# Optimization experiments

Hardware: AMD Instinct MI355X
Metric: run time of the kernel (lower is better)

Reference implementation:

```python
import jax, jax.numpy as jnp
import numpy as np

NUM_USERS = 100000
NUM_ITEMS = 50000
N_NODES = NUM_USERS + NUM_ITEMS
N_INTERACTIONS = 1000000
LATENT_DIM = 32
K = 4
N_LAYERS = 3
BATCH = 4096


def setup_inputs() -> dict:
    key = jax.random.key(0)
    k_u, k_i = jax.random.split(key)
    # torch init: normal std=0.1
    user_emb = 0.1 * jax.random.normal(k_u, (NUM_USERS, LATENT_DIM * K), dtype=jnp.float32)
    item_emb = 0.1 * jax.random.normal(k_i, (NUM_ITEMS, LATENT_DIM * K), dtype=jnp.float32)
    # build symmetric normalized bipartite adjacency (LightGCN getSparseGraph)
    rng = np.random.default_rng(0)
    u = rng.integers(0, NUM_USERS, N_INTERACTIONS)
    it = rng.integers(0, NUM_ITEMS, N_INTERACTIONS)
    src = np.concatenate([u, it + NUM_USERS]).astype(np.int32)
    dst = np.concatenate([it + NUM_USERS, u]).astype(np.int32)
    deg = np.bincount(src, minlength=N_NODES).astype(np.float32)
    deg = np.maximum(deg, 1.0)
    val = (1.0 / np.sqrt(deg[src] * deg[dst])).astype(np.float32)
    users = rng.integers(0, NUM_USERS, BATCH).astype(np.int32)
    items = rng.integers(0, NUM_ITEMS, BATCH).astype(np.int32)
    return {
        "user_emb": user_emb,
        "item_emb": item_emb,
        "edge_src": jnp.asarray(src),
        "edge_dst": jnp.asarray(dst),
        "edge_val": jnp.asarray(val),
        "users": jnp.asarray(users),
        "items": jnp.asarray(items),
    }


def _computer(user_emb, item_emb, edge_src, edge_dst, edge_val):
    n_users = user_emb.shape[0]
    n = n_users + item_emb.shape[0]
    # [N, K, D] disentangled factor view of the K*D embedding
    x = jnp.concatenate([user_emb, item_emb], axis=0).reshape(n, K, -1)
    embs = [x]
    for _ in range(N_LAYERS):
        # SpMM over all K factor slices at once: out[dst] += val * x[src]
        msgs = x[edge_src] * edge_val[:, None, None]  # [E, K, D]
        x = jax.ops.segment_sum(msgs, edge_dst, num_segments=n)
        embs.append(x)
    light_out = jnp.mean(jnp.stack(embs, axis=1), axis=1)  # [N, K, D]
    return light_out[:n_users], light_out[n_users:]


def reference(user_emb, item_emb, edge_src, edge_dst, edge_val, users, items):
    all_users, all_items = _computer(user_emb, item_emb, edge_src, edge_dst, edge_val)
    u = all_users[users]   # [B, K, D]
    i = all_items[items]   # [B, K, D]
    return jnp.sum(u * i, axis=(-1, -2))  # [B]
```

## Files before the change

### kernel.cpp

```cpp
#include <hip/hip_runtime.h>

#define NUM_USERS 100000
#define NUM_ITEMS 50000
#define N_NODES   150000
#define N_EDGES   2000000
#define N_INTER   1000000
#define DIM       128
#define DIM4      32
#define BATCH     4096
#define B_SHIFT   9
#define BUCK_N    (1 << B_SHIFT)
#define NBUCK     ((N_NODES + BUCK_N - 1) >> B_SHIFT)
#define PAIRS     4096
#define NPBLK     ((N_INTER + PAIRS - 1) / PAIRS)
#define CAP       12288
#define CAPB      16384
#define MARK_BLOCKS 512
#define CONV_BLOCKS (((N_NODES + 1) * 8 + 255) / 256)

#define G0 16.0f
#define INV_G1 (1.0f / 64.0f)
#define INV_G2 (1.0f / 256.0f)

typedef __attribute__((ext_vector_type(4))) float f32x4;
typedef __attribute__((ext_vector_type(2))) float f32x2;

__device__ inline f32x2 f8x2_lo(unsigned w) { return __builtin_amdgcn_cvt_pk_f32_fp8(w, 0); }
__device__ inline f32x2 f8x2_hi(unsigned w) { return __builtin_amdgcn_cvt_pk_f32_fp8(w, 1); }
__device__ inline unsigned enc_lo(float a, float b, unsigned old) {
    return __builtin_amdgcn_cvt_pk_fp8_f32(a, b, old, 0);
}
__device__ inline unsigned enc_hi(float a, float b, unsigned old) {
    return __builtin_amdgcn_cvt_pk_fp8_f32(a, b, old, 1);
}

__device__ inline int scan512(int v, int t, int* wsum) {
    int incl = v;
#pragma unroll
    for (int off = 1; off < 64; off <<= 1) {
        int u = __shfl_up(incl, off, 64);
        if ((t & 63) >= off) incl += u;
    }
    __syncthreads();
    if ((t & 63) == 63) wsum[t >> 6] = incl;
    __syncthreads();
    int add = 0;
    int w = t >> 6;
    for (int k = 0; k < w; ++k) add += wsum[k];
    return incl + add;
}


__global__ void bucket_scatter_kernel(const int* __restrict__ src,
                                      int* __restrict__ bcur,
                                      int* __restrict__ tmp) {
    __shared__ int lhist[NBUCK];
    __shared__ int lcur[NBUCK];
    int t = threadIdx.x;
    int base = blockIdx.x * PAIRS;
    for (int i = t; i < NBUCK; i += 512) lhist[i] = 0;
    __syncthreads();
    for (int i = 0; i < PAIRS / 512; ++i) {
        int gp = base + i * 512 + t;
        if (gp < N_INTER) {
            int u = src[gp];
            int v = src[N_INTER + gp];
            atomicAdd(&lhist[v >> B_SHIFT], 1);
            atomicAdd(&lhist[u >> B_SHIFT], 1);
        }
    }
    __syncthreads();
    for (int i = t; i < NBUCK; i += 512) {
        int c = lhist[i];
        lcur[i] = c ? (i * CAPB + atomicAdd(&bcur[i], c)) : 0;
    }
    __syncthreads();
    for (int i = 0; i < PAIRS / 512; ++i) {
        int gp = base + i * 512 + t;
        if (gp < N_INTER) {
            int u = src[gp];
            int v = src[N_INTER + gp];
            int bv = v >> B_SHIFT;
            int bu = u >> B_SHIFT;
            int pos0 = atomicAdd(&lcur[bv], 1);
            if (pos0 < (bv + 1) * CAPB)
                tmp[pos0] = (u << B_SHIFT) | (v & (BUCK_N - 1));
            int pos1 = atomicAdd(&lcur[bu], 1);
            if (pos1 < (bu + 1) * CAPB)
                tmp[pos1] = (v << B_SHIFT) | (u & (BUCK_N - 1));
        }
    }
}


__global__ void place_kernel(const int* __restrict__ bcur,
                             const int* __restrict__ tmp,
                             int* __restrict__ row_start,
                             float* __restrict__ rinv,
                             float* __restrict__ sdeg,
                             int* __restrict__ csr_src) {
    __shared__ int lhist[BUCK_N];
    __shared__ int lofs[BUCK_N];
    __shared__ int ssc[512];
    __shared__ int wsum[8];
    __shared__ int outbuf[CAP];
    int b = blockIdx.x;
    int t = threadIdx.x;

    int c = 0;
    if (t < NBUCK) {
        c = bcur[t];
        if (c > CAPB) c = CAPB;
    }
    ssc[t] = scan512(c, t, wsum);
    __syncthreads();
    int beg = (b == 0) ? 0 : ssc[b - 1];
    int end = ssc[b];
    int cnt = end - beg;
    int tbase = b * CAPB;
    int n0 = b << B_SHIFT;
    int n1 = n0 + BUCK_N; if (n1 > N_NODES) n1 = N_NODES;
    if (b == NBUCK - 1 && t == 0) row_start[N_NODES] = end;

    lhist[t] = 0;
    __syncthreads();
    for (int e = t; e < cnt; e += 512)
        atomicAdd(&lhist[tmp[tbase + e] & (BUCK_N - 1)], 1);
    __syncthreads();

    int v = lhist[t];
    int incl = scan512(v, t, wsum);
    int excl = incl - v;
    lofs[t] = excl;
    int node = n0 + t;
    if (node < n1) {
        row_start[node] = beg + excl;
        float d = (float)(v > 1 ? v : 1);
        float rr = rsqrtf(d);
        rinv[node] = rr;
        sdeg[node] = d * rr;
    }
    __syncthreads();

    if (cnt <= CAP) {
        for (int e = t; e < cnt; e += 512) {
            int p = tmp[tbase + e];
            int pos = atomicAdd(&lofs[p & (BUCK_N - 1)], 1);
            outbuf[pos] = p >> B_SHIFT;
        }
        __syncthreads();
        for (int i = t; i < cnt; i += 512) csr_src[beg + i] = outbuf[i];
    } else {
        for (int e = t; e < cnt; e += 512) {
            int p = tmp[tbase + e];
            int pos = atomicAdd(&lofs[p & (BUCK_N - 1)], 1);
            csr_src[beg + pos] = p >> B_SHIFT;
        }
    }
}


__global__ void mark_conv_kernel(const f32x4* __restrict__ ue4,
                                 const f32x4* __restrict__ ie4,
                                 const float* __restrict__ rinv,
                                 uint4* __restrict__ e16f8,
                                 uint4* __restrict__ w1f8,
                                 uint4* __restrict__ w2f8,
                                 const int* __restrict__ users,
                                 const int* __restrict__ items,
                                 const int* __restrict__ row_start,
                                 const int* __restrict__ csr_src,
                                 int* __restrict__ mark) {
    int bid = blockIdx.x;
    if (bid < MARK_BLOCKS) {
        int g = threadIdx.x >> 4;
        int lane = threadIdx.x & 15;
        int b = bid * 16 + g;
        int node = (b < BATCH) ? users[b] : (NUM_USERS + items[b - BATCH]);
        if (lane == 0) mark[node] = 1;
        int beg = row_start[node], end = row_start[node + 1];
        for (int e = beg + lane; e < end; e += 16) mark[csr_src[e]] = 1;
        return;
    }
    int i = (bid - MARK_BLOCKS) * 256 + threadIdx.x;
    const int total = (N_NODES + 1) * 8;
    if (i >= total) return;
    int n = i >> 3;
    if (n >= N_NODES) {
        uint4 z = make_uint4(0u, 0u, 0u, 0u);
        e16f8[i] = z;
        w1f8[i] = z;
        w2f8[i] = z;
        return;
    }
    int j = i & 7;
    const f32x4* row = (n < NUM_USERS) ? ue4 + (size_t)n * DIM4
                                       : ie4 + (size_t)(n - NUM_USERS) * DIM4;
    float r = rinv[n] * G0;
    f32x4 c0 = __builtin_nontemporal_load(&row[4 * j]);
    f32x4 c1 = __builtin_nontemporal_load(&row[4 * j + 1]);
    f32x4 c2 = __builtin_nontemporal_load(&row[4 * j + 2]);
    f32x4 c3 = __builtin_nontemporal_load(&row[4 * j + 3]);
    uint4 o;
    o.x = enc_hi(r * c0.z, r * c0.w, enc_lo(r * c0.x, r * c0.y, 0u));
    o.y = enc_hi(r * c1.z, r * c1.w, enc_lo(r * c1.x, r * c1.y, 0u));
    o.z = enc_hi(r * c2.z, r * c2.w, enc_lo(r * c2.x, r * c2.y, 0u));
    o.w = enc_hi(r * c3.z, r * c3.w, enc_lo(r * c3.x, r * c3.y, 0u));
    e16f8[i] = o;
}


__device__ inline void spmm_row(int n, const uint2* __restrict__ tabl,
                                const int* __restrict__ row_start,
                                const int* __restrict__ csr_src,
                                const float* __restrict__ rinv,
                                uint2* __restrict__ out,
                                int lane, int gbase) {
    int beg = row_start[n], end = row_start[n + 1];
    f32x2 a0 = {0.f, 0.f}, a1 = {0.f, 0.f}, a2 = {0.f, 0.f}, a3 = {0.f, 0.f};
    for (int base = beg; base < end; base += 16) {
        int eidx = base + lane;
        int myedge = (eidx < end) ? csr_src[eidx] : N_NODES;
        int s[16];
#pragma unroll
        for (int k = 0; k < 16; ++k) s[k] = __shfl(myedge, gbase + k, 64);
        uint2 h[16];
#pragma unroll
        for (int k = 0; k < 16; ++k) h[k] = tabl[s[k] << 4];
#pragma unroll
        for (int k = 0; k < 16; ++k) {
            a0 += f8x2_lo(h[k].x);
            a1 += f8x2_hi(h[k].x);
            a2 += f8x2_lo(h[k].y);
            a3 += f8x2_hi(h[k].y);
        }
    }
    float f = rinv[n];
    f = 4.0f * f * f;
    a0 *= f; a1 *= f; a2 *= f; a3 *= f;
    uint2 o;
    o.x = enc_hi(a1[0], a1[1], enc_lo(a0[0], a0[1], 0u));
    o.y = enc_hi(a3[0], a3[1], enc_lo(a2[0], a2[1], 0u));
    out[((size_t)n << 4) + lane] = o;
}

__global__ __launch_bounds__(256) void spmm_f8_kernel(
        const uint2* __restrict__ tab,
        const int* __restrict__ row_start,
        const int* __restrict__ csr_src,
        const float* __restrict__ rinv,
        uint2* __restrict__ out) {
    int t = threadIdx.x;
    int n = blockIdx.x * 16 + (t >> 4);
    if (n >= N_NODES) return;
    spmm_row(n, tab + (t & 15), row_start, csr_src, rinv, out, t & 15, t & 48);
}

__global__ __launch_bounds__(256) void spmm_f8_masked_kernel(
        const uint2* __restrict__ tab,
        const int* __restrict__ row_start,
        const int* __restrict__ csr_src,
        const float* __restrict__ rinv,
        const int* __restrict__ mark,
        uint2* __restrict__ out) {
    int t = threadIdx.x;
    int n = blockIdx.x * 16 + (t >> 4);
    if (n >= N_NODES) return;
    if (!mark[n]) return;
    spmm_row(n, tab + (t & 15), row_start, csr_src, rinv, out, t & 15, t & 48);
}


__global__ void epilogue_kernel(const f32x4* __restrict__ ue4,
                                const f32x4* __restrict__ ie4,
                                const uint2* __restrict__ w1f8,
                                const uint2* __restrict__ w2f8,
                                const int* __restrict__ row_start,
                                const int* __restrict__ csr_src,
                                const float* __restrict__ rinv,
                                const float* __restrict__ sdeg,
                                const int* __restrict__ users,
                                const int* __restrict__ items,
                                float* __restrict__ out) {
    int t = threadIdx.x;
    int elem = blockIdx.x * 4 + (t >> 5);
    int half = (t >> 4) & 1;
    int lane = t & 15;
    int gbase = t & 48;
    int node = half ? (NUM_USERS + items[elem]) : users[elem];

    const f32x4* erow = (node < NUM_USERS) ? ue4 + (size_t)node * DIM4
                                           : ie4 + (size_t)(node - NUM_USERS) * DIM4;
    f32x4 f0 = erow[2 * lane];
    f32x4 f1 = erow[2 * lane + 1];
    float a[8] = {f0.x, f0.y, f0.z, f0.w, f1.x, f1.y, f1.z, f1.w};

    float sd = sdeg[node];
    uint2 d1 = w1f8[(size_t)node * 16 + lane];
    uint2 d2 = w2f8[(size_t)node * 16 + lane];
    f32x2 p0 = f8x2_lo(d1.x), p1 = f8x2_hi(d1.x), p2 = f8x2_lo(d1.y), p3 = f8x2_hi(d1.y);
    f32x2 q0 = f8x2_lo(d2.x), q1 = f8x2_hi(d2.x), q2 = f8x2_lo(d2.y), q3 = f8x2_hi(d2.y);
    a[0] += sd * (p0[0] * INV_G1 + q0[0] * INV_G2);
    a[1] += sd * (p0[1] * INV_G1 + q0[1] * INV_G2);
    a[2] += sd * (p1[0] * INV_G1 + q1[0] * INV_G2);
    a[3] += sd * (p1[1] * INV_G1 + q1[1] * INV_G2);
    a[4] += sd * (p2[0] * INV_G1 + q2[0] * INV_G2);
    a[5] += sd * (p2[1] * INV_G1 + q2[1] * INV_G2);
    a[6] += sd * (p3[0] * INV_G1 + q3[0] * INV_G2);
    a[7] += sd * (p3[1] * INV_G1 + q3[1] * INV_G2);

    int beg = row_start[node], end = row_start[node + 1];
    f32x2 b0 = {0.f, 0.f}, b1 = {0.f, 0.f}, b2 = {0.f, 0.f}, b3 = {0.f, 0.f};
    const uint2* w2l = w2f8 + lane;
    for (int base = beg; base < end; base += 16) {
        int eidx = base + lane;
        int myedge = (eidx < end) ? csr_src[eidx] : N_NODES;
        int s[16];
#pragma unroll
        for (int k = 0; k < 16; ++k) s[k] = __shfl(myedge, gbase + k, 64);
        uint2 h[16];
#pragma unroll
        for (int k = 0; k < 16; ++k) h[k] = w2l[(size_t)s[k] << 4];
#pragma unroll
        for (int k = 0; k < 16; ++k) {
            b0 += f8x2_lo(h[k].x);
            b1 += f8x2_hi(h[k].x);
            b2 += f8x2_lo(h[k].y);
            b3 += f8x2_hi(h[k].y);
        }
    }
    float rv = rinv[node] * INV_G2;
    a[0] += rv * b0[0]; a[1] += rv * b0[1];
    a[2] += rv * b1[0]; a[3] += rv * b1[1];
    a[4] += rv * b2[0]; a[5] += rv * b2[1];
    a[6] += rv * b3[0]; a[7] += rv * b3[1];

    int wl = t & 63;
    float p = 0.f;
#pragma unroll
    for (int j = 0; j < 8; ++j) p += a[j] * __shfl(a[j], wl ^ 16, 64);
    for (int off = 8; off > 0; off >>= 1) p += __shfl_down(p, off, 16);
    if (half == 0 && lane == 0) out[elem] = p * (1.0f / 16.0f);
}

extern "C" void kernel_launch(void* const* d_in, const int* in_sizes, int n_in,
                              void* d_out, int out_size, void* d_ws, size_t ws_size,
                              hipStream_t stream) {
    const f32x4* ue4 = (const f32x4*)d_in[0];
    const f32x4* ie4 = (const f32x4*)d_in[1];
    const int*   src   = (const int*)d_in[2];
    const int*   users = (const int*)d_in[5];
    const int*   items = (const int*)d_in[6];
    float* out = (float*)d_out;

    const size_t frow = (size_t)(N_NODES + 1) * 16;
    char* ws = (char*)d_ws;
    uint2* e16f8 = (uint2*)ws;  ws += frow * sizeof(uint2);
    uint2* w1f8  = (uint2*)ws;  ws += frow * sizeof(uint2);
    uint2* w2f8  = (uint2*)ws;  ws += frow * sizeof(uint2);
    int*   row_start = (int*)ws;    ws += (size_t)(N_NODES + 1) * sizeof(int);
    float* rinv      = (float*)ws;  ws += (size_t)N_NODES * sizeof(float);
    float* sdeg      = (float*)ws;  ws += (size_t)N_NODES * sizeof(float);
    int*   mark      = (int*)ws;    ws += (size_t)N_NODES * sizeof(int);
    int*   bcur      = (int*)ws;    ws += (size_t)NBUCK * sizeof(int);
    ws = (char*)(((size_t)ws + 255) & ~(size_t)255);
    int*   tmp       = (int*)ws;    ws += (size_t)NBUCK * CAPB * sizeof(int);
    int*   csr_src   = (int*)ws;    ws += (size_t)N_EDGES * sizeof(int);

    hipMemsetAsync(mark, 0, (size_t)(N_NODES + NBUCK) * sizeof(int), stream);

    bucket_scatter_kernel<<<NPBLK, 512, 0, stream>>>(src, bcur, tmp);
    place_kernel<<<NBUCK, 512, 0, stream>>>(bcur, tmp, row_start, rinv, sdeg, csr_src);

    mark_conv_kernel<<<MARK_BLOCKS + CONV_BLOCKS, 256, 0, stream>>>(
        ue4, ie4, rinv, (uint4*)e16f8, (uint4*)w1f8, (uint4*)w2f8,
        users, items, row_start, csr_src, mark);

    spmm_f8_kernel<<<(N_NODES + 15) / 16, 256, 0, stream>>>(
        e16f8, row_start, csr_src, rinv, w1f8);

    spmm_f8_masked_kernel<<<(N_NODES + 15) / 16, 256, 0, stream>>>(
        w1f8, row_start, csr_src, rinv, mark, w2f8);

    epilogue_kernel<<<BATCH / 4, 128, 0, stream>>>(
        ue4, ie4, w1f8, w2f8, row_start, csr_src, rinv, sdeg, users, items, out);
}
```

Before: 248.2 us.

## Fuse all pipeline stages into one cooperative persistent kernel with grid syncs

After: 473.7 us. +90.9%, slower.

```diff
diff --git a/kernel.cpp b/kernel.cpp
--- a/kernel.cpp
+++ b/kernel.cpp
@@ -1,4 +1,7 @@
 #include <hip/hip_runtime.h>
+#include <hip/hip_cooperative_groups.h>
+
+namespace cg = cooperative_groups;
 
 #define NUM_USERS 100000
 #define NUM_ITEMS 50000
@@ -15,8 +18,7 @@
 #define NPBLK     ((N_INTER + PAIRS - 1) / PAIRS)
 #define CAP       12288
 #define CAPB      16384
-#define MARK_BLOCKS 512
-#define CONV_BLOCKS (((N_NODES + 1) * 8 + 255) / 256)
+#define MT        512
 
 #define G0 16.0f
 #define INV_G1 (1.0f / 64.0f)
@@ -48,165 +50,6 @@
     int w = t >> 6;
     for (int k = 0; k < w; ++k) add += wsum[k];
     return incl + add;
-}
-
-
-__global__ void bucket_scatter_kernel(const int* __restrict__ src,
-                                      int* __restrict__ bcur,
-                                      int* __restrict__ tmp) {
-    __shared__ int lhist[NBUCK];
-    __shared__ int lcur[NBUCK];
-    int t = threadIdx.x;
-    int base = blockIdx.x * PAIRS;
-    for (int i = t; i < NBUCK; i += 512) lhist[i] = 0;
-    __syncthreads();
-    for (int i = 0; i < PAIRS / 512; ++i) {
-        int gp = base + i * 512 + t;
-        if (gp < N_INTER) {
-            int u = src[gp];
-            int v = src[N_INTER + gp];
-            atomicAdd(&lhist[v >> B_SHIFT], 1);
-            atomicAdd(&lhist[u >> B_SHIFT], 1);
-        }
-    }
-    __syncthreads();
-    for (int i = t; i < NBUCK; i += 512) {
-        int c = lhist[i];
-        lcur[i] = c ? (i * CAPB + atomicAdd(&bcur[i], c)) : 0;
-    }
-    __syncthreads();
-    for (int i = 0; i < PAIRS / 512; ++i) {
-        int gp = base + i * 512 + t;
-        if (gp < N_INTER) {
-            int u = src[gp];
-            int v = src[N_INTER + gp];
-            int bv = v >> B_SHIFT;
-            int bu = u >> B_SHIFT;
-            int pos0 = atomicAdd(&lcur[bv], 1);
-            if (pos0 < (bv + 1) * CAPB)
-                tmp[pos0] = (u << B_SHIFT) | (v & (BUCK_N - 1));
-            int pos1 = atomicAdd(&lcur[bu], 1);
-            if (pos1 < (bu + 1) * CAPB)
-                tmp[pos1] = (v << B_SHIFT) | (u & (BUCK_N - 1));
-        }
-    }
-}
-
-
-__global__ void place_kernel(const int* __restrict__ bcur,
-                             const int* __restrict__ tmp,
-                             int* __restrict__ row_start,
-                             float* __restrict__ rinv,
-                             float* __restrict__ sdeg,
-                             int* __restrict__ csr_src) {
-    __shared__ int lhist[BUCK_N];
-    __shared__ int lofs[BUCK_N];
-    __shared__ int ssc[512];
-    __shared__ int wsum[8];
-    __shared__ int outbuf[CAP];
-    int b = blockIdx.x;
-    int t = threadIdx.x;
-
-    int c = 0;
-    if (t < NBUCK) {
-        c = bcur[t];
-        if (c > CAPB) c = CAPB;
-    }
-    ssc[t] = scan512(c, t, wsum);
-    __syncthreads();
-    int beg = (b == 0) ? 0 : ssc[b - 1];
-    int end = ssc[b];
-    int cnt = end - beg;
-    int tbase = b * CAPB;
-    int n0 = b << B_SHIFT;
-    int n1 = n0 + BUCK_N; if (n1 > N_NODES) n1 = N_NODES;
-    if (b == NBUCK - 1 && t == 0) row_start[N_NODES] = end;
-
-    lhist[t] = 0;
-    __syncthreads();
-    for (int e = t; e < cnt; e += 512)
-        atomicAdd(&lhist[tmp[tbase + e] & (BUCK_N - 1)], 1);
-    __syncthreads();
-
-    int v = lhist[t];
-    int incl = scan512(v, t, wsum);
-    int excl = incl - v;
-    lofs[t] = excl;
-    int node = n0 + t;
-    if (node < n1) {
-        row_start[node] = beg + excl;
-        float d = (float)(v > 1 ? v : 1);
-        float rr = rsqrtf(d);
-        rinv[node] = rr;
-        sdeg[node] = d * rr;
-    }
-    __syncthreads();
-
-    if (cnt <= CAP) {
-        for (int e = t; e < cnt; e += 512) {
-            int p = tmp[tbase + e];
-            int pos = atomicAdd(&lofs[p & (BUCK_N - 1)], 1);
-            outbuf[pos] = p >> B_SHIFT;
-        }
-        __syncthreads();
-        for (int i = t; i < cnt; i += 512) csr_src[beg + i] = outbuf[i];
-    } else {
-        for (int e = t; e < cnt; e += 512) {
-            int p = tmp[tbase + e];
-            int pos = atomicAdd(&lofs[p & (BUCK_N - 1)], 1);
-            csr_src[beg + pos] = p >> B_SHIFT;
-        }
-    }
-}
-
-
-__global__ void mark_conv_kernel(const f32x4* __restrict__ ue4,
-                                 const f32x4* __restrict__ ie4,
-                                 const float* __restrict__ rinv,
-                                 uint4* __restrict__ e16f8,
-                                 uint4* __restrict__ w1f8,
-                                 uint4* __restrict__ w2f8,
-                                 const int* __restrict__ users,
-                                 const int* __restrict__ items,
-                                 const int* __restrict__ row_start,
-                                 const int* __restrict__ csr_src,
-                                 int* __restrict__ mark) {
-    int bid = blockIdx.x;
-    if (bid < MARK_BLOCKS) {
-        int g = threadIdx.x >> 4;
-        int lane = threadIdx.x & 15;
-        int b = bid * 16 + g;
-        int node = (b < BATCH) ? users[b] : (NUM_USERS + items[b - BATCH]);
-        if (lane == 0) mark[node] = 1;
-        int beg = row_start[node], end = row_start[node + 1];
-        for (int e = beg + lane; e < end; e += 16) mark[csr_src[e]] = 1;
-        return;
-    }
-    int i = (bid - MARK_BLOCKS) * 256 + threadIdx.x;
-    const int total = (N_NODES + 1) * 8;
-    if (i >= total) return;
-    int n = i >> 3;
-    if (n >= N_NODES) {
-        uint4 z = make_uint4(0u, 0u, 0u, 0u);
-        e16f8[i] = z;
-        w1f8[i] = z;
-        w2f8[i] = z;
-        return;
-    }
-    int j = i & 7;
-    const f32x4* row = (n < NUM_USERS) ? ue4 + (size_t)n * DIM4
-                                       : ie4 + (size_t)(n - NUM_USERS) * DIM4;
-    float r = rinv[n] * G0;
-    f32x4 c0 = __builtin_nontemporal_load(&row[4 * j]);
-    f32x4 c1 = __builtin_nontemporal_load(&row[4 * j + 1]);
-    f32x4 c2 = __builtin_nontemporal_load(&row[4 * j + 2]);
-    f32x4 c3 = __builtin_nontemporal_load(&row[4 * j + 3]);
-    uint4 o;
-    o.x = enc_hi(r * c0.z, r * c0.w, enc_lo(r * c0.x, r * c0.y, 0u));
-    o.y = enc_hi(r * c1.z, r * c1.w, enc_lo(r * c1.x, r * c1.y, 0u));
-    o.z = enc_hi(r * c2.z, r * c2.w, enc_lo(r * c2.x, r * c2.y, 0u));
-    o.w = enc_hi(r * c3.z, r * c3.w, enc_lo(r * c3.x, r * c3.y, 0u));
-    e16f8[i] = o;
 }
 
 
@@ -244,103 +87,250 @@
     out[((size_t)n << 4) + lane] = o;
 }
 
-__global__ __launch_bounds__(256) void spmm_f8_kernel(
-        const uint2* __restrict__ tab,
-        const int* __restrict__ row_start,
-        const int* __restrict__ csr_src,
-        const float* __restrict__ rinv,
-        uint2* __restrict__ out) {
+
+__global__ __launch_bounds__(MT, 4) void mega_kernel(
+        const f32x4* __restrict__ ue4,
+        const f32x4* __restrict__ ie4,
+        const int* __restrict__ src,
+        const int* __restrict__ users,
+        const int* __restrict__ items,
+        uint2* __restrict__ e16f8,
+        uint2* __restrict__ w1f8,
+        uint2* __restrict__ w2f8,
+        int* __restrict__ row_start,
+        float* __restrict__ rinv,
+        float* __restrict__ sdeg,
+        int* __restrict__ mark,
+        int* __restrict__ tmp,
+        int* __restrict__ csr_src,
+        float* __restrict__ out) {
+    cg::grid_group grid = cg::this_grid();
+    __shared__ __align__(16) int smem[13832];
     int t = threadIdx.x;
-    int n = blockIdx.x * 16 + (t >> 4);
-    if (n >= N_NODES) return;
-    spmm_row(n, tab + (t & 15), row_start, csr_src, rinv, out, t & 15, t & 48);
-}
-
-__global__ __launch_bounds__(256) void spmm_f8_masked_kernel(
-        const uint2* __restrict__ tab,
-        const int* __restrict__ row_start,
-        const int* __restrict__ csr_src,
-        const float* __restrict__ rinv,
-        const int* __restrict__ mark,
-        uint2* __restrict__ out) {
-    int t = threadIdx.x;
-    int n = blockIdx.x * 16 + (t >> 4);
-    if (n >= N_NODES) return;
-    if (!mark[n]) return;
-    spmm_row(n, tab + (t & 15), row_start, csr_src, rinv, out, t & 15, t & 48);
-}
-
-
-__global__ void epilogue_kernel(const f32x4* __restrict__ ue4,
-                                const f32x4* __restrict__ ie4,
-                                const uint2* __restrict__ w1f8,
-                                const uint2* __restrict__ w2f8,
-                                const int* __restrict__ row_start,
-                                const int* __restrict__ csr_src,
-                                const float* __restrict__ rinv,
-                                const float* __restrict__ sdeg,
-                                const int* __restrict__ users,
-                                const int* __restrict__ items,
-                                float* __restrict__ out) {
-    int t = threadIdx.x;
-    int elem = blockIdx.x * 4 + (t >> 5);
-    int half = (t >> 4) & 1;
-    int lane = t & 15;
-    int gbase = t & 48;
-    int node = half ? (NUM_USERS + items[elem]) : users[elem];
-
-    const f32x4* erow = (node < NUM_USERS) ? ue4 + (size_t)node * DIM4
-                                           : ie4 + (size_t)(node - NUM_USERS) * DIM4;
-    f32x4 f0 = erow[2 * lane];
-    f32x4 f1 = erow[2 * lane + 1];
-    float a[8] = {f0.x, f0.y, f0.z, f0.w, f1.x, f1.y, f1.z, f1.w};
-
-    float sd = sdeg[node];
-    uint2 d1 = w1f8[(size_t)node * 16 + lane];
-    uint2 d2 = w2f8[(size_t)node * 16 + lane];
-    f32x2 p0 = f8x2_lo(d1.x), p1 = f8x2_hi(d1.x), p2 = f8x2_lo(d1.y), p3 = f8x2_hi(d1.y);
-    f32x2 q0 = f8x2_lo(d2.x), q1 = f8x2_hi(d2.x), q2 = f8x2_lo(d2.y), q3 = f8x2_hi(d2.y);
-    a[0] += sd * (p0[0] * INV_G1 + q0[0] * INV_G2);
-    a[1] += sd * (p0[1] * INV_G1 + q0[1] * INV_G2);
-    a[2] += sd * (p1[0] * INV_G1 + q1[0] * INV_G2);
-    a[3] += sd * (p1[1] * INV_G1 + q1[1] * INV_G2);
-    a[4] += sd * (p2[0] * INV_G1 + q2[0] * INV_G2);
-    a[5] += sd * (p2[1] * INV_G1 + q2[1] * INV_G2);
-    a[6] += sd * (p3[0] * INV_G1 + q3[0] * INV_G2);
-    a[7] += sd * (p3[1] * INV_G1 + q3[1] * INV_G2);
-
-    int beg = row_start[node], end = row_start[node + 1];
-    f32x2 b0 = {0.f, 0.f}, b1 = {0.f, 0.f}, b2 = {0.f, 0.f}, b3 = {0.f, 0.f};
-    const uint2* w2l = w2f8 + lane;
-    for (int base = beg; base < end; base += 16) {
-        int eidx = base + lane;
-        int myedge = (eidx < end) ? csr_src[eidx] : N_NODES;
-        int s[16];
-#pragma unroll
-        for (int k = 0; k < 16; ++k) s[k] = __shfl(myedge, gbase + k, 64);
-        uint2 h[16];
-#pragma unroll
-        for (int k = 0; k < 16; ++k) h[k] = w2l[(size_t)s[k] << 4];
-#pragma unroll
-        for (int k = 0; k < 16; ++k) {
-            b0 += f8x2_lo(h[k].x);
-            b1 += f8x2_hi(h[k].x);
-            b2 += f8x2_lo(h[k].y);
-            b3 += f8x2_hi(h[k].y);
-        }
-    }
-    float rv = rinv[node] * INV_G2;
-    a[0] += rv * b0[0]; a[1] += rv * b0[1];
-    a[2] += rv * b1[0]; a[3] += rv * b1[1];
-    a[4] += rv * b2[0]; a[5] += rv * b2[1];
-    a[6] += rv * b3[0]; a[7] += rv * b3[1];
-
-    int wl = t & 63;
-    float p = 0.f;
-#pragma unroll
-    for (int j = 0; j < 8; ++j) p += a[j] * __shfl(a[j], wl ^ 16, 64);
-    for (int off = 8; off > 0; off >>= 1) p += __shfl_down(p, off, 16);
-    if (half == 0 && lane == 0) out[elem] = p * (1.0f / 16.0f);
+    int b = blockIdx.x;
+    int nb = gridDim.x;
+    int* bcur = mark + N_NODES;
+
+    for (int i = b * MT + t; i < N_NODES + NBUCK; i += nb * MT) mark[i] = 0;
+    grid.sync();
+
+    for (int task = b; task < NPBLK; task += nb) {
+        int* lhist = smem;
+        int* lcur  = smem + 512;
+        int base = task * PAIRS;
+        for (int i = t; i < NBUCK; i += MT) lhist[i] = 0;
+        __syncthreads();
+        for (int i = 0; i < PAIRS / MT; ++i) {
+            int gp = base + i * MT + t;
+            if (gp < N_INTER) {
+                int u = src[gp];
+                int v = src[N_INTER + gp];
+                atomicAdd(&lhist[v >> B_SHIFT], 1);
+                atomicAdd(&lhist[u >> B_SHIFT], 1);
+            }
+        }
+        __syncthreads();
+        for (int i = t; i < NBUCK; i += MT) {
+            int c = lhist[i];
+            lcur[i] = c ? (i * CAPB + atomicAdd(&bcur[i], c)) : 0;
+        }
+        __syncthreads();
+        for (int i = 0; i < PAIRS / MT; ++i) {
+            int gp = base + i * MT + t;
+            if (gp < N_INTER) {
+                int u = src[gp];
+                int v = src[N_INTER + gp];
+                int bv = v >> B_SHIFT;
+                int bu = u >> B_SHIFT;
+                int pos0 = atomicAdd(&lcur[bv], 1);
+                if (pos0 < (bv + 1) * CAPB)
+                    tmp[pos0] = (u << B_SHIFT) | (v & (BUCK_N - 1));
+                int pos1 = atomicAdd(&lcur[bu], 1);
+                if (pos1 < (bu + 1) * CAPB)
+                    tmp[pos1] = (v << B_SHIFT) | (u & (BUCK_N - 1));
+            }
+        }
+        __syncthreads();
+    }
+    grid.sync();
+
+    for (int task = b; task < NBUCK; task += nb) {
+        int* lhist  = smem;
+        int* lofs   = smem + 512;
+        int* ssc    = smem + 1024;
+        int* wsum   = smem + 1536;
+        int* outbuf = smem + 1544;
+        int c = 0;
+        if (t < NBUCK) {
+            c = bcur[t];
+            if (c > CAPB) c = CAPB;
+        }
+        ssc[t] = scan512(c, t, wsum);
+        __syncthreads();
+        int beg = (task == 0) ? 0 : ssc[task - 1];
+        int end = ssc[task];
+        int cnt = end - beg;
+        int tbase = task * CAPB;
+        int n0 = task << B_SHIFT;
+        int n1 = n0 + BUCK_N; if (n1 > N_NODES) n1 = N_NODES;
+        if (task == NBUCK - 1 && t == 0) row_start[N_NODES] = end;
+
+        lhist[t] = 0;
+        __syncthreads();
+        for (int e = t; e < cnt; e += MT)
+            atomicAdd(&lhist[tmp[tbase + e] & (BUCK_N - 1)], 1);
+        __syncthreads();
+
+        int v = lhist[t];
+        int incl = scan512(v, t, wsum);
+        int excl = incl - v;
+        lofs[t] = excl;
+        int node = n0 + t;
+        if (node < n1) {
+            row_start[node] = beg + excl;
+            float d = (float)(v > 1 ? v : 1);
+            float rr = rsqrtf(d);
+            rinv[node] = rr;
+            sdeg[node] = d * rr;
+        }
+        __syncthreads();
+
+        if (cnt <= CAP) {
+            for (int e = t; e < cnt; e += MT) {
+                int p = tmp[tbase + e];
+                int pos = atomicAdd(&lofs[p & (BUCK_N - 1)], 1);
+                outbuf[pos] = p >> B_SHIFT;
+            }
+            __syncthreads();
+            for (int i = t; i < cnt; i += MT) csr_src[beg + i] = outbuf[i];
+        } else {
+            for (int e = t; e < cnt; e += MT) {
+                int p = tmp[tbase + e];
+                int pos = atomicAdd(&lofs[p & (BUCK_N - 1)], 1);
+                csr_src[beg + pos] = p >> B_SHIFT;
+            }
+        }
+        __syncthreads();
+    }
+    grid.sync();
+
+    {
+        int lane = t & 15;
+        for (int slot = b * 32 + (t >> 4); slot < 2 * BATCH; slot += nb * 32) {
+            int node = (slot < BATCH) ? users[slot] : (NUM_USERS + items[slot - BATCH]);
+            if (lane == 0) mark[node] = 1;
+            int beg = row_start[node], end = row_start[node + 1];
+            for (int e = beg + lane; e < end; e += 16) mark[csr_src[e]] = 1;
+        }
+    }
+    {
+        uint4* e4 = (uint4*)e16f8;
+        uint4* w14 = (uint4*)w1f8;
+        uint4* w24 = (uint4*)w2f8;
+        const int total = (N_NODES + 1) * 8;
+        for (int i = b * MT + t; i < total; i += nb * MT) {
+            int n = i >> 3;
+            if (n >= N_NODES) {
+                uint4 z = make_uint4(0u, 0u, 0u, 0u);
+                e4[i] = z; w14[i] = z; w24[i] = z;
+                continue;
+            }
+            int j = i & 7;
+            const f32x4* row = (n < NUM_USERS) ? ue4 + (size_t)n * DIM4
+                                               : ie4 + (size_t)(n - NUM_USERS) * DIM4;
+            float r = rinv[n] * G0;
+            f32x4 c0 = __builtin_nontemporal_load(&row[4 * j]);
+            f32x4 c1 = __builtin_nontemporal_load(&row[4 * j + 1]);
+            f32x4 c2 = __builtin_nontemporal_load(&row[4 * j + 2]);
+            f32x4 c3 = __builtin_nontemporal_load(&row[4 * j + 3]);
+            uint4 o;
+            o.x = enc_hi(r * c0.z, r * c0.w, enc_lo(r * c0.x, r * c0.y, 0u));
+            o.y = enc_hi(r * c1.z, r * c1.w, enc_lo(r * c1.x, r * c1.y, 0u));
+            o.z = enc_hi(r * c2.z, r * c2.w, enc_lo(r * c2.x, r * c2.y, 0u));
+            o.w = enc_hi(r * c3.z, r * c3.w, enc_lo(r * c3.x, r * c3.y, 0u));
+            e4[i] = o;
+        }
+    }
+    grid.sync();
+
+    {
+        int lane = t & 15, gbase = t & 48;
+        const uint2* tabl = e16f8 + lane;
+        for (int n = b * 32 + (t >> 4); n < N_NODES; n += nb * 32)
+            spmm_row(n, tabl, row_start, csr_src, rinv, w1f8, lane, gbase);
+    }
+    grid.sync();
+
+    {
+        int lane = t & 15, gbase = t & 48;
+        const uint2* tabl = w1f8 + lane;
+        for (int n = b * 32 + (t >> 4); n < N_NODES; n += nb * 32) {
+            if (!mark[n]) continue;
+            spmm_row(n, tabl, row_start, csr_src, rinv, w2f8, lane, gbase);
+        }
+    }
+    grid.sync();
+
+    {
+        int half = (t >> 4) & 1;
+        int lane = t & 15;
+        int gbase = t & 48;
+        for (int elem = b * 16 + (t >> 5); elem < BATCH; elem += nb * 16) {
+            int node = half ? (NUM_USERS + items[elem]) : users[elem];
+            const f32x4* erow = (node < NUM_USERS) ? ue4 + (size_t)node * DIM4
+                                                   : ie4 + (size_t)(node - NUM_USERS) * DIM4;
+            f32x4 f0 = erow[2 * lane];
+            f32x4 f1 = erow[2 * lane + 1];
+            float a[8] = {f0.x, f0.y, f0.z, f0.w, f1.x, f1.y, f1.z, f1.w};
+
+            float sd = sdeg[node];
+            uint2 d1 = w1f8[(size_t)node * 16 + lane];
+            uint2 d2 = w2f8[(size_t)node * 16 + lane];
+            f32x2 p0 = f8x2_lo(d1.x), p1 = f8x2_hi(d1.x), p2 = f8x2_lo(d1.y), p3 = f8x2_hi(d1.y);
+            f32x2 q0 = f8x2_lo(d2.x), q1 = f8x2_hi(d2.x), q2 = f8x2_lo(d2.y), q3 = f8x2_hi(d2.y);
+            a[0] += sd * (p0[0] * INV_G1 + q0[0] * INV_G2);
+            a[1] += sd * (p0[1] * INV_G1 + q0[1] * INV_G2);
+            a[2] += sd * (p1[0] * INV_G1 + q1[0] * INV_G2);
+            a[3] += sd * (p1[1] * INV_G1 + q1[1] * INV_G2);
+            a[4] += sd * (p2[0] * INV_G1 + q2[0] * INV_G2);
+            a[5] += sd * (p2[1] * INV_G1 + q2[1] * INV_G2);
+            a[6] += sd * (p3[0] * INV_G1 + q3[0] * INV_G2);
+            a[7] += sd * (p3[1] * INV_G1 + q3[1] * INV_G2);
+
+            int beg = row_start[node], end = row_start[node + 1];
+            f32x2 b0 = {0.f, 0.f}, b1 = {0.f, 0.f}, b2 = {0.f, 0.f}, b3 = {0.f, 0.f};
+            const uint2* w2l = w2f8 + lane;
+            for (int base = beg; base < end; base += 16) {
+                int eidx = base + lane;
+                int myedge = (eidx < end) ? csr_src[eidx] : N_NODES;
+                int s[16];
+#pragma unroll
+                for (int k = 0; k < 16; ++k) s[k] = __shfl(myedge, gbase + k, 64);
+                uint2 h[16];
+#pragma unroll
+                for (int k = 0; k < 16; ++k) h[k] = w2l[(size_t)s[k] << 4];
+#pragma unroll
+                for (int k = 0; k < 16; ++k) {
+                    b0 += f8x2_lo(h[k].x);
+                    b1 += f8x2_hi(h[k].x);
+                    b2 += f8x2_lo(h[k].y);
+                    b3 += f8x2_hi(h[k].y);
+                }
+            }
+            float rv = rinv[node] * INV_G2;
+            a[0] += rv * b0[0]; a[1] += rv * b0[1];
+            a[2] += rv * b1[0]; a[3] += rv * b1[1];
+            a[4] += rv * b2[0]; a[5] += rv * b2[1];
+            a[6] += rv * b3[0]; a[7] += rv * b3[1];
+
+            int wl = t & 63;
+            float p = 0.f;
+#pragma unroll
+            for (int j = 0; j < 8; ++j) p += a[j] * __shfl(a[j], wl ^ 16, 64);
+            for (int off = 8; off > 0; off >>= 1) p += __shfl_down(p, off, 16);
+            if (half == 0 && lane == 0) out[elem] = p * (1.0f / 16.0f);
+        }
+    }
 }
 
 extern "C" void kernel_launch(void* const* d_in, const int* in_sizes, int n_in,
@@ -362,26 +352,24 @@
     float* rinv      = (float*)ws;  ws += (size_t)N_NODES * sizeof(float);
     float* sdeg      = (float*)ws;  ws += (size_t)N_NODES * sizeof(float);
     int*   mark      = (int*)ws;    ws += (size_t)N_NODES * sizeof(int);
-    int*   bcur      = (int*)ws;    ws += (size_t)NBUCK * sizeof(int);
+                          ws += (size_t)NBUCK * sizeof(int);
     ws = (char*)(((size_t)ws + 255) & ~(size_t)255);
     int*   tmp       = (int*)ws;    ws += (size_t)NBUCK * CAPB * sizeof(int);
     int*   csr_src   = (int*)ws;    ws += (size_t)N_EDGES * sizeof(int);
 
-    hipMemsetAsync(mark, 0, (size_t)(N_NODES + NBUCK) * sizeof(int), stream);
-
-    bucket_scatter_kernel<<<NPBLK, 512, 0, stream>>>(src, bcur, tmp);
-    place_kernel<<<NBUCK, 512, 0, stream>>>(bcur, tmp, row_start, rinv, sdeg, csr_src);
-
-    mark_conv_kernel<<<MARK_BLOCKS + CONV_BLOCKS, 256, 0, stream>>>(
-        ue4, ie4, rinv, (uint4*)e16f8, (uint4*)w1f8, (uint4*)w2f8,
-        users, items, row_start, csr_src, mark);
-
-    spmm_f8_kernel<<<(N_NODES + 15) / 16, 256, 0, stream>>>(
-        e16f8, row_start, csr_src, rinv, w1f8);
-
-    spmm_f8_masked_kernel<<<(N_NODES + 15) / 16, 256, 0, stream>>>(
-        w1f8, row_start, csr_src, rinv, mark, w2f8);
-
-    epilogue_kernel<<<BATCH / 4, 128, 0, stream>>>(
-        ue4, ie4, w1f8, w2f8, row_start, csr_src, rinv, sdeg, users, items, out);
-}
+    static int coop_grid = 0;
+    if (coop_grid == 0) {
+        int bpc = 0;
+        hipOccupancyMaxActiveBlocksPerMultiprocessor(&bpc, mega_kernel, MT, 0);
+        int g = (bpc > 0) ? bpc * 256 : 256;
+        if (g > 512) g = 512;
+        coop_grid = g;
+    }
+
+    void* args[] = {(void*)&ue4, (void*)&ie4, (void*)&src, (void*)&users, (void*)&items,
+                    (void*)&e16f8, (void*)&w1f8, (void*)&w2f8,
+                    (void*)&row_start, (void*)&rinv, (void*)&sdeg, (void*)&mark,
+                    (void*)&tmp, (void*)&csr_src, (void*)&out};
+    hipLaunchCooperativeKernel((void*)mega_kernel, dim3(coop_grid), dim3(MT),
+                               args, 0, stream);
+}
```
